# Kernel optimization log

Hardware: AMD Instinct MI355X
Metric: run time of the kernel (lower is better)

## Reference

```python
import jax, jax.numpy as jnp
import numpy as np

NHEAD = 8
TEMP = 1.0
LAMB = 1.0
G_MIN = 1e-3


def _linear(x, w, b):
    # torch nn.Linear convention: w is (out, in)
    return x @ w.T + b


def _ln(x, s, b):
    m = x.mean(-1, keepdims=True)
    v = ((x - m) ** 2).mean(-1, keepdims=True)
    return (x - m) / jnp.sqrt(v + 1e-5) * s + b


def _gate(x, w, b):
    # UncertaintyGate, gate_mode='mu_times_evi'
    nig = _linear(x, w, b)  # [B, L, 4]
    mu = nig[..., 0]
    v = jax.nn.softplus(nig[..., 1]) + 1e-6
    alpha = jax.nn.softplus(nig[..., 2]) + 1.0 + 1e-6
    beta = jax.nn.softplus(nig[..., 3]) + 1e-6
    sigma_e2 = beta / (v * (alpha - 1.0))
    g = jax.nn.sigmoid(mu) * jnp.exp(-LAMB * sigma_e2)
    return jnp.clip(g, G_MIN, 1.0)  # [B, L]


def _cross_attn(q, k, v, gate, mask):
    B, Lq, D = q.shape
    Lk = k.shape[1]
    hd = D // NHEAD
    q = q.reshape(B, Lq, NHEAD, hd).transpose(0, 2, 1, 3)
    k = k.reshape(B, Lk, NHEAD, hd).transpose(0, 2, 1, 3)
    v = v.reshape(B, Lk, NHEAD, hd).transpose(0, 2, 1, 3)
    scores = jnp.einsum('bhqd,bhkd->bhqk', q, k) / jnp.sqrt(jnp.float32(hd))
    scores = scores + jnp.log(gate + 1e-9)[:, None, None, :]  # per-key log-gate bias
    scores = jnp.where(mask[:, None, None, :] == 0, -1e9, scores)
    attn = jax.nn.softmax(scores / TEMP, axis=-1)
    out = jnp.einsum('bhqk,bhkd->bhqd', attn, v)
    return out.transpose(0, 2, 1, 3).reshape(B, Lq, D)


def _ffn(x, w1, b1, w2, b2):
    return _linear(jax.nn.gelu(_linear(x, w1, b1), approximate=False), w2, b2)


def setup_inputs() -> dict:
    key = jax.random.key(0)
    ks = iter(jax.random.split(key, 64))
    D, B, Ld, Lp = 512, 16, 256, 1024
    def w(shape, s=0.02):
        return jax.random.normal(next(ks), shape, jnp.float32) * s
    inp = {
        'h_d': jax.random.normal(next(ks), (B, Ld, D), jnp.float32),
        'h_p': jax.random.normal(next(ks), (B, Lp, D), jnp.float32),
        'gd_w': w((4, D)), 'gd_b': jnp.zeros((4,), jnp.float32),
        'gp_w': w((4, D)), 'gp_b': jnp.zeros((4,), jnp.float32),
        'wqd_w': w((D, D)), 'wqd_b': jnp.zeros((D,), jnp.float32),
        'wkp_w': w((D, D)), 'wkp_b': jnp.zeros((D,), jnp.float32),
        'wvp_w': w((D, D)), 'wvp_b': jnp.zeros((D,), jnp.float32),
        'wqp_w': w((D, D)), 'wqp_b': jnp.zeros((D,), jnp.float32),
        'wkd_w': w((D, D)), 'wkd_b': jnp.zeros((D,), jnp.float32),
        'wvd_w': w((D, D)), 'wvd_b': jnp.zeros((D,), jnp.float32),
        'od_w': w((D, D)), 'od_b': jnp.zeros((D,), jnp.float32),
        'op_w': w((D, D)), 'op_b': jnp.zeros((D,), jnp.float32),
        'fd1_w': w((4 * D, D)), 'fd1_b': jnp.zeros((4 * D,), jnp.float32),
        'fd2_w': w((D, 4 * D)), 'fd2_b': jnp.zeros((D,), jnp.float32),
        'fp1_w': w((4 * D, D)), 'fp1_b': jnp.zeros((4 * D,), jnp.float32),
        'fp2_w': w((D, 4 * D)), 'fp2_b': jnp.zeros((D,), jnp.float32),
        'nd1_s': jnp.ones((D,), jnp.float32), 'nd1_b': jnp.zeros((D,), jnp.float32),
        'nd2_s': jnp.ones((D,), jnp.float32), 'nd2_b': jnp.zeros((D,), jnp.float32),
        'np1_s': jnp.ones((D,), jnp.float32), 'np1_b': jnp.zeros((D,), jnp.float32),
        'np2_s': jnp.ones((D,), jnp.float32), 'np2_b': jnp.zeros((D,), jnp.float32),
        'mask_d': jnp.ones((B, Ld), jnp.int32),
        'mask_p': jnp.ones((B, Lp), jnp.int32),
    }
    return inp


def reference(h_d, h_p, gd_w, gd_b, gp_w, gp_b, wqd_w, wqd_b, wkp_w, wkp_b,
              wvp_w, wvp_b, wqp_w, wqp_b, wkd_w, wkd_b, wvd_w, wvd_b,
              od_w, od_b, op_w, op_b, fd1_w, fd1_b, fd2_w, fd2_b,
              fp1_w, fp1_b, fp2_w, fp2_b, nd1_s, nd1_b, nd2_s, nd2_b,
              np1_s, np1_b, np2_s, np2_b, mask_d, mask_p):
    # gates are computed from the ORIGINAL inputs
    g_d = _gate(h_d, gd_w, gd_b)
    g_p = _gate(h_p, gp_w, gp_b)
    # drug attends to protein
    attn_d = _cross_attn(_linear(h_d, wqd_w, wqd_b),
                         _linear(h_p, wkp_w, wkp_b),
                         _linear(h_p, wvp_w, wvp_b), g_p, mask_p)
    h_d = _ln(h_d + _linear(attn_d, od_w, od_b), nd1_s, nd1_b)
    # protein attends to UPDATED drug (matches original control flow)
    attn_p = _cross_attn(_linear(h_p, wqp_w, wqp_b),
                         _linear(h_d, wkd_w, wkd_b),
                         _linear(h_d, wvd_w, wvd_b), g_d, mask_d)
    h_p = _ln(h_p + _linear(attn_p, op_w, op_b), np1_s, np1_b)
    h_d = _ln(h_d + _ffn(h_d, fd1_w, fd1_b, fd2_w, fd2_b), nd2_s, nd2_b)
    h_p = _ln(h_p + _ffn(h_p, fp1_w, fp1_b, fp2_w, fp2_b), np2_s, np2_b)
    return (h_d, h_p)
```

## Files before the change

kernel.cpp:

```cpp
#include <hip/hip_runtime.h>

typedef float f32x4 __attribute__((ext_vector_type(4)));
typedef short bfrag __attribute__((ext_vector_type(8)));
typedef short s16x8 __attribute__((ext_vector_type(8)));
typedef unsigned short u16;

__device__ __forceinline__ u16 f2bf(float f) {
  union { float f; unsigned u; } x; x.f = f;
  unsigned r = x.u + 0x7fffu + ((x.u >> 16) & 1u);
  return (u16)(r >> 16);
}
__device__ __forceinline__ float bf2f(u16 v) {
  union { unsigned u; float f; } x; x.u = ((unsigned)v) << 16;
  return x.f;
}

__device__ __forceinline__ void g2l16(const void* g, void* l) {
  void* gnc = const_cast<void*>(g);
  __builtin_amdgcn_global_load_lds((__attribute__((address_space(1))) void*)gnc,
                                   (__attribute__((address_space(3))) void*)l, 16, 0, 0);
}

__device__ __forceinline__ f32x4 mfma16(bfrag a, bfrag b, f32x4 c) {
  asm volatile("v_mfma_f32_16x16x32_bf16 %0, %1, %2, %0" : "+v"(c) : "v"(a), "v"(b));
  return c;
}

__device__ __forceinline__ float wred_sum(float s) {
  #pragma unroll
  for (int o = 32; o; o >>= 1) s += __shfl_xor(s, o);
  return s;
}

__device__ __forceinline__ float gelu_f(float v) {
  return 0.5f * v * (1.f + erff(v * 0.70710678118f));
}

struct CvtArgs {
  const float* s[14];
  u16* d[14];
  int eb[14];
};

__global__ __launch_bounds__(256) void cvt_all(CvtArgs a) {
  const int blk = blockIdx.x;
  int base = 0;
  const float* sp = a.s[0];
  u16* dp = a.d[0];
  #pragma unroll
  for (int i = 0; i < 13; ++i) {
    if (blk >= a.eb[i]) { base = a.eb[i]; sp = a.s[i + 1]; dp = a.d[i + 1]; }
  }
  const size_t gi = ((size_t)(blk - base) * 256 + threadIdx.x) * 4;
  float4 f = *(const float4*)(sp + gi);
  ushort4 o;
  o.x = f2bf(f.x); o.y = f2bf(f.y); o.z = f2bf(f.z); o.w = f2bf(f.w);
  *(ushort4*)(dp + gi) = o;
}

__global__ __launch_bounds__(512) void biascat_k(
    const float* __restrict__ bkp, const float* __restrict__ bvp,
    const float* __restrict__ bqp, const float* __restrict__ bkd,
    const float* __restrict__ bvd, float* __restrict__ bp3,
    float* __restrict__ bd2) {
  int t = threadIdx.x;
  bp3[t] = bkp[t];
  bp3[512 + t] = bvp[t];
  bp3[1024 + t] = bqp[t];
  bd2[t] = bkd[t];
  bd2[512 + t] = bvd[t];
}

__device__ __forceinline__ float softplus_s(float x) {
  return fmaxf(x, 0.f) + log1pf(expf(-fabsf(x)));
}

__global__ __launch_bounds__(256) void gate_k(
    const float* __restrict__ hd, const float* __restrict__ hp,
    const float* __restrict__ wd, const float* __restrict__ bd,
    const float* __restrict__ wp, const float* __restrict__ bp,
    float* __restrict__ lgd, float* __restrict__ lgp, int mdTok) {
  const int lane = threadIdx.x & 63, wv = threadIdx.x >> 6;
  size_t tok = (size_t)blockIdx.x * 4 + wv;
  const float* h; const float* w4; const float* b4; float* lg;
  if (tok < (size_t)mdTok) { h = hd; w4 = wd; b4 = bd; lg = lgd; }
  else { h = hp; w4 = wp; b4 = bp; lg = lgp; tok -= mdTok; }
  const float* x = h + tok * 512;
  float s0 = 0.f, s1 = 0.f, s2 = 0.f, s3 = 0.f;
  #pragma unroll
  for (int i = 0; i < 8; ++i) {
    int c = (i << 6) + lane;
    float xv = x[c];
    s0 += xv * w4[c];
    s1 += xv * w4[512 + c];
    s2 += xv * w4[1024 + c];
    s3 += xv * w4[1536 + c];
  }
  s0 = wred_sum(s0); s1 = wred_sum(s1); s2 = wred_sum(s2); s3 = wred_sum(s3);
  if (lane == 0) {
    float mu = s0 + b4[0];
    float va = softplus_s(s1 + b4[1]) + 1e-6f;
    float al = softplus_s(s2 + b4[2]) + 1.f + 1e-6f;
    float be = softplus_s(s3 + b4[3]) + 1e-6f;
    float se2 = be / (va * (al - 1.f));
    float g = (1.f / (1.f + expf(-mu))) * expf(-se2);
    g = fminf(fmaxf(g, 1e-3f), 1.f);
    lg[tok] = logf(g + 1e-9f);
  }
}

template <int OUT>
__global__ __launch_bounds__(256) void ln_k(const u16* __restrict__ res,
                                            const u16* __restrict__ y,
                                            const float* __restrict__ sc,
                                            const float* __restrict__ bi,
                                            void* __restrict__ outv) {
  const int lane = threadIdx.x & 63, w = threadIdx.x >> 6;
  const size_t row = (size_t)blockIdx.x * 4 + w;
  const int c0 = lane * 8;
  float v[8];
  s16x8 yv = *(const s16x8*)(y + row * 512 + c0);
  s16x8 rv = *(const s16x8*)(res + row * 512 + c0);
  float s = 0.f;
  #pragma unroll
  for (int i = 0; i < 8; ++i) {
    v[i] = bf2f((u16)rv[i]) + bf2f((u16)yv[i]);
    s += v[i];
  }
  s = wred_sum(s);
  float m = s * (1.f / 512.f);
  float s2 = 0.f;
  #pragma unroll
  for (int i = 0; i < 8; ++i) { float d = v[i] - m; s2 += d * d; }
  s2 = wred_sum(s2);
  float inv = rsqrtf(s2 * (1.f / 512.f) + 1e-5f);
  float4 sc0 = *(const float4*)(sc + c0), sc1 = *(const float4*)(sc + c0 + 4);
  float4 bi0 = *(const float4*)(bi + c0), bi1 = *(const float4*)(bi + c0 + 4);
  float scv[8] = {sc0.x, sc0.y, sc0.z, sc0.w, sc1.x, sc1.y, sc1.z, sc1.w};
  float biv[8] = {bi0.x, bi0.y, bi0.z, bi0.w, bi1.x, bi1.y, bi1.z, bi1.w};
  float o[8];
  #pragma unroll
  for (int i = 0; i < 8; ++i) o[i] = (v[i] - m) * inv * scv[i] + biv[i];
  if constexpr (OUT == 0) {
    float* of = (float*)outv + row * 512 + c0;
    *(float4*)of = float4{o[0], o[1], o[2], o[3]};
    *(float4*)(of + 4) = float4{o[4], o[5], o[6], o[7]};
  } else {
    s16x8 ov;
    #pragma unroll
    for (int i = 0; i < 8; ++i) ov[i] = (short)f2bf(o[i]);
    *(s16x8*)((u16*)outv + row * 512 + c0) = ov;
  }
}

template <int KT>
__global__ __launch_bounds__(256) void flash_k(
    const u16* __restrict__ Q, const u16* __restrict__ Kv,
    const u16* __restrict__ Vt, const float* __restrict__ logg,
    const int* __restrict__ mask, u16* __restrict__ Out,
    int Lq, int Lk, float scale) {
  __shared__ __align__(16) u16 Kl[KT * 64];
  __shared__ __align__(16) u16 Vl[64 * KT];
  __shared__ __align__(16) u16 Pl[64 * (KT + 8)];
  const int tid = threadIdx.x;
  const int lane = tid & 63, wv = tid >> 6;
  const int lr = lane & 15, lg4 = lane >> 4;
  const int bh = blockIdx.z;
  const int b = bh >> 3, h = bh & 7;
  const int q0 = blockIdx.x * 64;

  bfrag af[2];
  {
    const u16* qrow = Q + (size_t)(b * Lq + q0 + wv * 16 + lr) * 512 + h * 64;
    af[0] = *(const bfrag*)(qrow + lg4 * 8);
    af[1] = *(const bfrag*)(qrow + 32 + lg4 * 8);
  }
  float mreg[4] = {-3e38f, -3e38f, -3e38f, -3e38f};
  float lreg[4] = {0.f, 0.f, 0.f, 0.f};
  f32x4 Oa[4] = {};
  const float* lgb = logg + (size_t)b * Lk;
  const int* mkb = mask + (size_t)b * Lk;

  const int NKT = Lk / KT;
  for (int t = 0; t < NKT; ++t) {
    const int k0 = t * KT;
    __syncthreads();
    {
      const char* kb = (const char*)(Kv + (size_t)(b * Lk + k0) * 512 + h * 64);
      #pragma unroll
      for (int r = 0; r < KT / 32; ++r) {
        int o = r * 4096 + tid * 16;
        int rr = o >> 7, cd = (o >> 4) & 7;
        int cs = cd ^ (rr & 7);
        g2l16(kb + (size_t)rr * 1024 + cs * 16, (char*)Kl + o);
      }
      const char* vb = (const char*)(Vt + (size_t)bh * 64 * Lk + k0);
      #pragma unroll
      for (int r = 0; r < KT / 32; ++r) {
        int o = r * 4096 + tid * 16;
        int rr = o >> 8, cd = (o >> 4) & 15;
        int cs = (cd & 8) | ((cd & 7) ^ (rr & 7));
        g2l16(vb + (size_t)rr * (Lk * 2) + cs * 16, (char*)Vl + o);
      }
    }
    __syncthreads();

    f32x4 sa[KT / 16];
    #pragma unroll
    for (int n = 0; n < KT / 16; ++n) {
      sa[n] = f32x4{0.f, 0.f, 0.f, 0.f};
      int row = n * 16 + lr;
      #pragma unroll
      for (int ks = 0; ks < 2; ++ks) {
        bfrag kf = *(const bfrag*)(Kl + row * 64 + (((ks * 4 + lg4) ^ (row & 7)) * 8));
        sa[n] = mfma16(af[ks], kf, sa[n]);
      }
    }
    asm volatile("s_nop 7\n\ts_nop 7");

    float pv[KT / 16][4];
    float nm[4] = {-3e38f, -3e38f, -3e38f, -3e38f};
    #pragma unroll
    for (int n = 0; n < KT / 16; ++n) {
      int kk = k0 + n * 16 + lr;
      float lgv = lgb[kk];
      int mkv = mkb[kk];
      #pragma unroll
      for (int e = 0; e < 4; ++e) {
        float tv = mkv ? fmaf(sa[n][e], scale, lgv) : -1e9f;
        pv[n][e] = tv;
        nm[e] = fmaxf(nm[e], tv);
      }
    }
    float fac[4], rs[4];
    #pragma unroll
    for (int e = 0; e < 4; ++e) {
      nm[e] = fmaxf(nm[e], __shfl_xor(nm[e], 1));
      nm[e] = fmaxf(nm[e], __shfl_xor(nm[e], 2));
      nm[e] = fmaxf(nm[e], __shfl_xor(nm[e], 4));
      nm[e] = fmaxf(nm[e], __shfl_xor(nm[e], 8));
      nm[e] = fmaxf(nm[e], mreg[e]);
      fac[e] = __expf(mreg[e] - nm[e]);
      mreg[e] = nm[e];
      rs[e] = 0.f;
    }
    #pragma unroll
    for (int n = 0; n < KT / 16; ++n)
      #pragma unroll
      for (int e = 0; e < 4; ++e) {
        float p = __expf(pv[n][e] - nm[e]);
        pv[n][e] = p;
        rs[e] += p;
      }
    #pragma unroll
    for (int e = 0; e < 4; ++e) {
      rs[e] += __shfl_xor(rs[e], 1);
      rs[e] += __shfl_xor(rs[e], 2);
      rs[e] += __shfl_xor(rs[e], 4);
      rs[e] += __shfl_xor(rs[e], 8);
      lreg[e] = lreg[e] * fac[e] + rs[e];
    }
    #pragma unroll
    for (int n2 = 0; n2 < 4; ++n2)
      #pragma unroll
      for (int e = 0; e < 4; ++e) Oa[n2][e] *= fac[e];

    {
      int prow = wv * 16 + lg4 * 4;
      #pragma unroll
      for (int n = 0; n < KT / 16; ++n)
        #pragma unroll
        for (int e = 0; e < 4; ++e)
          Pl[(prow + e) * (KT + 8) + n * 16 + lr] = f2bf(pv[n][e]);
    }
    #pragma unroll
    for (int ks = 0; ks < KT / 32; ++ks) {
      bfrag pf = *(const bfrag*)(Pl + (wv * 16 + lr) * (KT + 8) + (ks * 4 + lg4) * 8);
      #pragma unroll
      for (int n2 = 0; n2 < 4; ++n2) {
        int vrow = n2 * 16 + lr;
        int ch = ks * 4 + lg4;
        int chs = (ch & 8) | ((ch & 7) ^ (vrow & 7));
        bfrag vf = *(const bfrag*)(Vl + vrow * KT + chs * 8);
        Oa[n2] = mfma16(pf, vf, Oa[n2]);
      }
    }
  }
  asm volatile("s_nop 7\n\ts_nop 7");

  float inv[4];
  #pragma unroll
  for (int e = 0; e < 4; ++e) inv[e] = 1.f / lreg[e];
  u16* ob = Out + (size_t)(b * Lq + q0 + wv * 16 + lg4 * 4) * 512 + h * 64;
  #pragma unroll
  for (int n2 = 0; n2 < 4; ++n2)
    #pragma unroll
    for (int e = 0; e < 4; ++e)
      ob[(size_t)e * 512 + n2 * 16 + lr] = f2bf(Oa[n2][e] * inv[e]);
}

template <int FM, int FN, int EPI>
__global__ __launch_bounds__(256) void gemm_k(
    const u16* __restrict__ A, const u16* __restrict__ W,
    const float* __restrict__ bias, void* __restrict__ C, void* __restrict__ C2,
    void* __restrict__ C3, int K, int lda, int ldw, int ldc, int NB, int TR) {
  constexpr int BM = 2 * FM * 16;
  constexpr int BN = 2 * FN * 16;
  __shared__ __align__(16) u16 Al[BM * 64];
  __shared__ __align__(16) u16 Wl[BN * 64];
  const int tid = threadIdx.x;
  const int qq = gridDim.x >> 3;
  const int wg = (blockIdx.x & 7) * qq + (blockIdx.x >> 3);
  const int bx = wg % NB, by = wg / NB;
  const int row0 = by * BM, col0 = bx * BN;
  const int lane = tid & 63, wv = tid >> 6;
  const int wr = wv >> 1, wc = wv & 1;
  const int rowW = wr * FM * 16, colW = wc * FN * 16;
  const int lr = lane & 15, lg4 = lane >> 4;

  const u16* aSrc[BM / 32];
  const u16* wSrc[BN / 32];
  int aDst[BM / 32], wDst[BN / 32];
  #pragma unroll
  for (int r = 0; r < BM / 32; ++r) {
    int o = r * 4096 + tid * 16;
    int arow = o >> 7, cd = (o >> 4) & 7, cs = cd ^ (arow & 7);
    aSrc[r] = A + (size_t)(row0 + arow) * lda + cs * 8;
    aDst[r] = o;
  }
  #pragma unroll
  for (int r = 0; r < BN / 32; ++r) {
    int o = r * 4096 + tid * 16;
    int wrow = o >> 7, cd = (o >> 4) & 7, cs = cd ^ (wrow & 7);
    wSrc[r] = W + (size_t)(col0 + wrow) * ldw + cs * 8;
    wDst[r] = o;
  }
  int aOff[FM][2], wOff[FN][2];
  #pragma unroll
  for (int m = 0; m < FM; ++m) {
    int rowi = rowW + m * 16 + lr;
    #pragma unroll
    for (int ks = 0; ks < 2; ++ks)
      aOff[m][ks] = rowi * 64 + (((ks * 4 + lg4) ^ (rowi & 7)) * 8);
  }
  #pragma unroll
  for (int n = 0; n < FN; ++n) {
    int rowi = colW + n * 16 + lr;
    #pragma unroll
    for (int ks = 0; ks < 2; ++ks)
      wOff[n][ks] = rowi * 64 + (((ks * 4 + lg4) ^ (rowi & 7)) * 8);
  }

  f32x4 acc[FM][FN] = {};

  for (int k0 = 0; k0 < K; k0 += 64) {
    #pragma unroll
    for (int r = 0; r < BM / 32; ++r) g2l16(aSrc[r] + k0, (char*)Al + aDst[r]);
    #pragma unroll
    for (int r = 0; r < BN / 32; ++r) g2l16(wSrc[r] + k0, (char*)Wl + wDst[r]);
    __syncthreads();
    #pragma unroll
    for (int ks = 0; ks < 2; ++ks) {
      bfrag af[FM], wf[FN];
      #pragma unroll
      for (int m = 0; m < FM; ++m) af[m] = *(const bfrag*)(Al + aOff[m][ks]);
      #pragma unroll
      for (int n = 0; n < FN; ++n) wf[n] = *(const bfrag*)(Wl + wOff[n][ks]);
      #pragma unroll
      for (int m = 0; m < FM; ++m)
        #pragma unroll
        for (int n = 0; n < FN; ++n) acc[m][n] = mfma16(af[m], wf[n], acc[m][n]);
    }
    if (k0 + 64 < K) __syncthreads();
  }
  asm volatile("s_nop 7\n\ts_nop 7\n\ts_nop 7");

  #pragma unroll
  for (int m = 0; m < FM; ++m) {
    #pragma unroll
    for (int n = 0; n < FN; ++n) {
      int rb = row0 + rowW + m * 16 + lg4 * 4;
      int c = col0 + colW + n * 16 + lr;
      float bv = bias[c];
      if constexpr (EPI == 1) {
        u16* Cu = (u16*)C;
        #pragma unroll
        for (int e = 0; e < 4; ++e)
          Cu[(size_t)(rb + e) * ldc + c] = f2bf(acc[m][n][e] + bv);
      } else if constexpr (EPI == 2) {
        u16* Cu = (u16*)C;
        #pragma unroll
        for (int e = 0; e < 4; ++e)
          Cu[(size_t)(rb + e) * ldc + c] = f2bf(gelu_f(acc[m][n][e] + bv));
      } else if constexpr (EPI == 4) {
        if (c < 512) {
          u16* Cu = (u16*)C;
          #pragma unroll
          for (int e = 0; e < 4; ++e)
            Cu[(size_t)(rb + e) * 512 + c] = f2bf(acc[m][n][e] + bv);
        } else if (c < 1024) {
          u16* Cu = (u16*)C2;
          int cl = c - 512;
          int b2 = rb / TR, j0 = rb - b2 * TR;
          int h2 = cl >> 6, dd = cl & 63;
          ushort4 pk;
          pk.x = f2bf(acc[m][n][0] + bv);
          pk.y = f2bf(acc[m][n][1] + bv);
          pk.z = f2bf(acc[m][n][2] + bv);
          pk.w = f2bf(acc[m][n][3] + bv);
          *(ushort4*)&Cu[(((size_t)b2 * 8 + h2) * 64 + dd) * TR + j0] = pk;
        } else {
          u16* Cu = (u16*)C3;
          int cl = c - 1024;
          #pragma unroll
          for (int e = 0; e < 4; ++e)
            Cu[(size_t)(rb + e) * 512 + cl] = f2bf(acc[m][n][e] + bv);
        }
      } else {
        if (c < 512) {
          u16* Cu = (u16*)C;
          #pragma unroll
          for (int e = 0; e < 4; ++e)
            Cu[(size_t)(rb + e) * ldc + c] = f2bf(acc[m][n][e] + bv);
        } else {
          u16* Cu = (u16*)C2;
          int cl = c - 512;
          int b2 = rb / TR, j0 = rb - b2 * TR;
          int h2 = cl >> 6, dd = cl & 63;
          ushort4 pk;
          pk.x = f2bf(acc[m][n][0] + bv);
          pk.y = f2bf(acc[m][n][1] + bv);
          pk.z = f2bf(acc[m][n][2] + bv);
          pk.w = f2bf(acc[m][n][3] + bv);
          *(ushort4*)&Cu[(((size_t)b2 * 8 + h2) * 64 + dd) * TR + j0] = pk;
        }
      }
    }
  }
}

extern "C" void kernel_launch(void* const* d_in, const int* in_sizes, int n_in,
                              void* d_out, int out_size, void* d_ws, size_t ws_size,
                              hipStream_t stream) {
  const float* h_d = (const float*)d_in[0];
  const float* h_p = (const float*)d_in[1];
  const float* gd_w = (const float*)d_in[2];
  const float* gd_b = (const float*)d_in[3];
  const float* gp_w = (const float*)d_in[4];
  const float* gp_b = (const float*)d_in[5];
  const float* wqd_w = (const float*)d_in[6];  const float* wqd_b = (const float*)d_in[7];
  const float* wkp_w = (const float*)d_in[8];  const float* wkp_b = (const float*)d_in[9];
  const float* wvp_w = (const float*)d_in[10]; const float* wvp_b = (const float*)d_in[11];
  const float* wqp_w = (const float*)d_in[12]; const float* wqp_b = (const float*)d_in[13];
  const float* wkd_w = (const float*)d_in[14]; const float* wkd_b = (const float*)d_in[15];
  const float* wvd_w = (const float*)d_in[16]; const float* wvd_b = (const float*)d_in[17];
  const float* od_w = (const float*)d_in[18];  const float* od_b = (const float*)d_in[19];
  const float* op_w = (const float*)d_in[20];  const float* op_b = (const float*)d_in[21];
  const float* fd1_w = (const float*)d_in[22]; const float* fd1_b = (const float*)d_in[23];
  const float* fd2_w = (const float*)d_in[24]; const float* fd2_b = (const float*)d_in[25];
  const float* fp1_w = (const float*)d_in[26]; const float* fp1_b = (const float*)d_in[27];
  const float* fp2_w = (const float*)d_in[28]; const float* fp2_b = (const float*)d_in[29];
  const float* nd1_s = (const float*)d_in[30]; const float* nd1_b = (const float*)d_in[31];
  const float* nd2_s = (const float*)d_in[32]; const float* nd2_b = (const float*)d_in[33];
  const float* np1_s = (const float*)d_in[34]; const float* np1_b = (const float*)d_in[35];
  const float* np2_s = (const float*)d_in[36]; const float* np2_b = (const float*)d_in[37];
  const int* mask_d = (const int*)d_in[38];
  const int* mask_p = (const int*)d_in[39];

  constexpr int B = 16, Ld = 256, Lp = 1024, D = 512, H = 8, F = 2048;
  constexpr int Md = B * Ld;
  constexpr int Mp = B * Lp;
  constexpr int BH = B * H;

  char* ws = (char*)d_ws;
  size_t off = 0;
  auto alloc = [&](size_t bytes) {
    size_t o = off;
    off += (bytes + 255) & ~(size_t)255;
    return o;
  };
  auto a16 = [&](size_t els) { return (u16*)(ws + alloc(els * 2)); };
  auto a32 = [&](size_t els) { return (float*)(ws + alloc(els * 4)); };

  u16* w_qd = a16((size_t)D * D);
  u16* w_kp = a16((size_t)D * D);
  u16* w_vp = a16((size_t)D * D);
  u16* w_qp = a16((size_t)D * D);
  u16* w_kd = a16((size_t)D * D);
  u16* w_vd = a16((size_t)D * D);
  u16* w_od = a16((size_t)D * D);
  u16* w_op = a16((size_t)D * D);
  u16* w_fd1 = a16((size_t)F * D);
  u16* w_fd2 = a16((size_t)F * D);
  u16* w_fp1 = a16((size_t)F * D);
  u16* w_fp2 = a16((size_t)F * D);

  u16* hd16 = a16((size_t)Md * D);
  u16* hd2_16 = a16((size_t)Md * D);
  u16* hp16 = a16((size_t)Mp * D);
  u16* qd16 = a16((size_t)Md * D);
  u16* kp16 = a16((size_t)Mp * D);
  u16* qp16 = a16((size_t)Mp * D);
  u16* vt16 = a16((size_t)Mp * D);
  u16* obuf16 = a16((size_t)Mp * D);
  u16* t16 = a16((size_t)Mp * F);
  float* logg_d = a32(Md);
  float* logg_p = a32(Mp);
  float* bp3 = a32(1536);
  float* bd2 = a32(1024);

  {
    CvtArgs a;
    const float* src[14] = {h_d, h_p, wqd_w, wkp_w, wvp_w, wqp_w, wkd_w,
                            wvd_w, od_w, op_w, fd1_w, fd2_w, fp1_w, fp2_w};
    u16* dst[14] = {hd16, hp16, w_qd, w_kp, w_vp, w_qp, w_kd,
                    w_vd, w_od, w_op, w_fd1, w_fd2, w_fp1, w_fp2};
    const int nelem[14] = {Md * D, Mp * D, D * D, D * D, D * D, D * D, D * D,
                           D * D, D * D, D * D, F * D, F * D, F * D, F * D};
    int pfx = 0;
    for (int i = 0; i < 14; ++i) {
      a.s[i] = src[i];
      a.d[i] = dst[i];
      pfx += nelem[i] / 1024;
      a.eb[i] = pfx;
    }
    cvt_all<<<pfx, 256, 0, stream>>>(a);
  }
  biascat_k<<<1, 512, 0, stream>>>(wkp_b, wvp_b, wqp_b, wkd_b, wvd_b, bp3, bd2);

  gate_k<<<(Md + Mp) / 4, 256, 0, stream>>>(h_d, h_p, gd_w, gd_b, gp_w, gp_b,
                                            logg_d, logg_p, Md);

  gemm_k<4, 4, 4><<<(Mp / 128) * (1536 / 128), 256, 0, stream>>>(
      hp16, w_kp, bp3, kp16, vt16, qp16, D, D, D, D, 1536 / 128, Lp);

  gemm_k<4, 4, 1><<<(Md / 128) * (D / 128), 256, 0, stream>>>(
      hd16, w_qd, wqd_b, qd16, nullptr, nullptr, D, D, D, D, D / 128, 0);

  flash_k<128><<<dim3(Ld / 64, 1, BH), 256, 0, stream>>>(
      qd16, kp16, vt16, logg_p, mask_p, qd16, Ld, Lp, 0.125f);

  gemm_k<4, 4, 1><<<(Md / 128) * (D / 128), 256, 0, stream>>>(
      qd16, w_od, od_b, obuf16, nullptr, nullptr, D, D, D, D, D / 128, 0);
  ln_k<1><<<Md / 4, 256, 0, stream>>>(hd16, obuf16, nd1_s, nd1_b, hd2_16);

  gemm_k<4, 4, 5><<<(Md / 128) * (1024 / 128), 256, 0, stream>>>(
      hd2_16, w_kd, bd2, qd16, vt16, nullptr, D, D, D, D, 1024 / 128, Ld);

  flash_k<128><<<dim3(Lp / 64, 1, BH), 256, 0, stream>>>(
      qp16, qd16, vt16, logg_d, mask_d, qp16, Lp, Ld, 0.125f);

  gemm_k<4, 4, 1><<<(Mp / 128) * (D / 128), 256, 0, stream>>>(
      qp16, w_op, op_b, obuf16, nullptr, nullptr, D, D, D, D, D / 128, 0);
  ln_k<1><<<Mp / 4, 256, 0, stream>>>(hp16, obuf16, np1_s, np1_b, hp16);

  gemm_k<4, 4, 2><<<(Md / 128) * (F / 128), 256, 0, stream>>>(
      hd2_16, w_fd1, fd1_b, t16, nullptr, nullptr, D, D, D, F, F / 128, 0);
  gemm_k<4, 4, 1><<<(Md / 128) * (D / 128), 256, 0, stream>>>(
      t16, w_fd2, fd2_b, obuf16, nullptr, nullptr, F, F, F, D, D / 128, 0);
  ln_k<0><<<Md / 4, 256, 0, stream>>>(hd2_16, obuf16, nd2_s, nd2_b, (float*)d_out);

  gemm_k<4, 4, 2><<<(Mp / 128) * (F / 128), 256, 0, stream>>>(
      hp16, w_fp1, fp1_b, t16, nullptr, nullptr, D, D, D, F, F / 128, 0);
  gemm_k<4, 4, 1><<<(Mp / 128) * (D / 128), 256, 0, stream>>>(
      t16, w_fp2, fp2_b, obuf16, nullptr, nullptr, F, F, F, D, D / 128, 0);
  ln_k<0><<<Mp / 4, 256, 0, stream>>>(hp16, obuf16, np2_s, np2_b,
                                      (float*)d_out + (size_t)Md * D);
}
```

Before: 396.5 us.

## Batch independent GEMMs into grouped launches and fuse final LayerNorms

Replaces the templated GEMM with a runtime descriptor-driven kernel that can run two independent GEMMs in one grid. Groups KVQ with Qd, Kd/Vd with the drug FFN1, and protein FFN1 with drug FFN2, and merges the two final LayerNorms into one launch. The aim is fewer launches and better CU fill on small GEMMs. It also shrinks the K-tile from 64 to 32 with a new swizzle, which means more barriers per K step, and moves the epilogue choice to runtime branches.

New measurement: 422.1 us. +6.5%, slower.

```diff
diff --git a/kernel.cpp b/kernel.cpp
--- a/kernel.cpp
+++ b/kernel.cpp
@@ -109,14 +109,10 @@
   }
 }
 
-template <int OUT>
-__global__ __launch_bounds__(256) void ln_k(const u16* __restrict__ res,
-                                            const u16* __restrict__ y,
-                                            const float* __restrict__ sc,
-                                            const float* __restrict__ bi,
-                                            void* __restrict__ outv) {
-  const int lane = threadIdx.x & 63, w = threadIdx.x >> 6;
-  const size_t row = (size_t)blockIdx.x * 4 + w;
+__device__ __forceinline__ void ln_body(const u16* res, const u16* y,
+                                        const float* sc, const float* bi,
+                                        void* outv, int fp32out, size_t row,
+                                        int lane) {
   const int c0 = lane * 8;
   float v[8];
   s16x8 yv = *(const s16x8*)(y + row * 512 + c0);
@@ -141,7 +137,7 @@
   float o[8];
   #pragma unroll
   for (int i = 0; i < 8; ++i) o[i] = (v[i] - m) * inv * scv[i] + biv[i];
-  if constexpr (OUT == 0) {
+  if (fp32out) {
     float* of = (float*)outv + row * 512 + c0;
     *(float4*)of = float4{o[0], o[1], o[2], o[3]};
     *(float4*)(of + 4) = float4{o[4], o[5], o[6], o[7]};
@@ -151,6 +147,31 @@
     for (int i = 0; i < 8; ++i) ov[i] = (short)f2bf(o[i]);
     *(s16x8*)((u16*)outv + row * 512 + c0) = ov;
   }
+}
+
+__global__ __launch_bounds__(256) void ln_k(const u16* __restrict__ res,
+                                            const u16* __restrict__ y,
+                                            const float* __restrict__ sc,
+                                            const float* __restrict__ bi,
+                                            u16* __restrict__ out) {
+  const int lane = threadIdx.x & 63, w = threadIdx.x >> 6;
+  const size_t row = (size_t)blockIdx.x * 4 + w;
+  ln_body(res, y, sc, bi, out, 0, row, lane);
+}
+
+__global__ __launch_bounds__(256) void lnf_k(
+    const u16* __restrict__ rd, const u16* __restrict__ yd,
+    const float* __restrict__ scd, const float* __restrict__ bid,
+    float* __restrict__ od,
+    const u16* __restrict__ rp, const u16* __restrict__ yp,
+    const float* __restrict__ scp, const float* __restrict__ bip,
+    float* __restrict__ op, int mdRows) {
+  const int lane = threadIdx.x & 63, w = threadIdx.x >> 6;
+  size_t row = (size_t)blockIdx.x * 4 + w;
+  if (row < (size_t)mdRows)
+    ln_body(rd, yd, scd, bid, od, 1, row, lane);
+  else
+    ln_body(rp, yp, scp, bip, op, 1, row - mdRows, lane);
 }
 
 template <int KT>
@@ -299,140 +320,123 @@
       ob[(size_t)e * 512 + n2 * 16 + lr] = f2bf(Oa[n2][e] * inv[e]);
 }
 
-template <int FM, int FN, int EPI>
-__global__ __launch_bounds__(256) void gemm_k(
-    const u16* __restrict__ A, const u16* __restrict__ W,
-    const float* __restrict__ bias, void* __restrict__ C, void* __restrict__ C2,
-    void* __restrict__ C3, int K, int lda, int ldw, int ldc, int NB, int TR) {
-  constexpr int BM = 2 * FM * 16;
-  constexpr int BN = 2 * FN * 16;
-  __shared__ __align__(16) u16 Al[BM * 64];
-  __shared__ __align__(16) u16 Wl[BN * 64];
+struct GemmDesc {
+  const u16* A;
+  const u16* W;
+  const float* bias;
+  u16 *C, *C2, *C3;
+  int K, lda, ldw, ldc, NB, TR, epi, nblocks;
+};
+
+__global__ __launch_bounds__(256) void gemm_k(GemmDesc d0, GemmDesc d1) {
+  __shared__ __align__(16) u16 Al[128 * 32];
+  __shared__ __align__(16) u16 Wl[128 * 32];
   const int tid = threadIdx.x;
   const int qq = gridDim.x >> 3;
-  const int wg = (blockIdx.x & 7) * qq + (blockIdx.x >> 3);
-  const int bx = wg % NB, by = wg / NB;
-  const int row0 = by * BM, col0 = bx * BN;
+  int wg = (blockIdx.x & 7) * qq + (blockIdx.x >> 3);
+  const GemmDesc& d = (wg < d0.nblocks) ? d0 : d1;
+  if (wg >= d0.nblocks) wg -= d0.nblocks;
+  const int bx = wg % d.NB, by = wg / d.NB;
+  const int row0 = by * 128, col0 = bx * 128;
   const int lane = tid & 63, wv = tid >> 6;
   const int wr = wv >> 1, wc = wv & 1;
-  const int rowW = wr * FM * 16, colW = wc * FN * 16;
+  const int rowW = wr * 64, colW = wc * 64;
   const int lr = lane & 15, lg4 = lane >> 4;
-
-  const u16* aSrc[BM / 32];
-  const u16* wSrc[BN / 32];
-  int aDst[BM / 32], wDst[BN / 32];
-  #pragma unroll
-  for (int r = 0; r < BM / 32; ++r) {
+  const int K = d.K;
+
+  const u16* aSrc[2];
+  const u16* wSrc[2];
+  int aDst[2], wDst[2];
+  #pragma unroll
+  for (int r = 0; r < 2; ++r) {
     int o = r * 4096 + tid * 16;
-    int arow = o >> 7, cd = (o >> 4) & 7, cs = cd ^ (arow & 7);
-    aSrc[r] = A + (size_t)(row0 + arow) * lda + cs * 8;
+    int row = o >> 6, cd = (o >> 4) & 3, cs = cd ^ ((row >> 1) & 3);
+    aSrc[r] = d.A + (size_t)(row0 + row) * d.lda + cs * 8;
+    wSrc[r] = d.W + (size_t)(col0 + row) * d.ldw + cs * 8;
     aDst[r] = o;
-  }
-  #pragma unroll
-  for (int r = 0; r < BN / 32; ++r) {
-    int o = r * 4096 + tid * 16;
-    int wrow = o >> 7, cd = (o >> 4) & 7, cs = cd ^ (wrow & 7);
-    wSrc[r] = W + (size_t)(col0 + wrow) * ldw + cs * 8;
     wDst[r] = o;
   }
-  int aOff[FM][2], wOff[FN][2];
-  #pragma unroll
-  for (int m = 0; m < FM; ++m) {
+  int aOff[4], wOff[4];
+  #pragma unroll
+  for (int m = 0; m < 4; ++m) {
     int rowi = rowW + m * 16 + lr;
-    #pragma unroll
-    for (int ks = 0; ks < 2; ++ks)
-      aOff[m][ks] = rowi * 64 + (((ks * 4 + lg4) ^ (rowi & 7)) * 8);
-  }
-  #pragma unroll
-  for (int n = 0; n < FN; ++n) {
-    int rowi = colW + n * 16 + lr;
-    #pragma unroll
-    for (int ks = 0; ks < 2; ++ks)
-      wOff[n][ks] = rowi * 64 + (((ks * 4 + lg4) ^ (rowi & 7)) * 8);
-  }
-
-  f32x4 acc[FM][FN] = {};
-
-  for (int k0 = 0; k0 < K; k0 += 64) {
-    #pragma unroll
-    for (int r = 0; r < BM / 32; ++r) g2l16(aSrc[r] + k0, (char*)Al + aDst[r]);
-    #pragma unroll
-    for (int r = 0; r < BN / 32; ++r) g2l16(wSrc[r] + k0, (char*)Wl + wDst[r]);
+    aOff[m] = rowi * 32 + ((lg4 ^ ((rowi >> 1) & 3)) * 8);
+    int rowj = colW + m * 16 + lr;
+    wOff[m] = rowj * 32 + ((lg4 ^ ((rowj >> 1) & 3)) * 8);
+  }
+
+  f32x4 acc[4][4] = {};
+
+  for (int k0 = 0; k0 < K; k0 += 32) {
+    #pragma unroll
+    for (int r = 0; r < 2; ++r) g2l16(aSrc[r] + k0, (char*)Al + aDst[r]);
+    #pragma unroll
+    for (int r = 0; r < 2; ++r) g2l16(wSrc[r] + k0, (char*)Wl + wDst[r]);
     __syncthreads();
-    #pragma unroll
-    for (int ks = 0; ks < 2; ++ks) {
-      bfrag af[FM], wf[FN];
-      #pragma unroll
-      for (int m = 0; m < FM; ++m) af[m] = *(const bfrag*)(Al + aOff[m][ks]);
-      #pragma unroll
-      for (int n = 0; n < FN; ++n) wf[n] = *(const bfrag*)(Wl + wOff[n][ks]);
-      #pragma unroll
-      for (int m = 0; m < FM; ++m)
-        #pragma unroll
-        for (int n = 0; n < FN; ++n) acc[m][n] = mfma16(af[m], wf[n], acc[m][n]);
-    }
-    if (k0 + 64 < K) __syncthreads();
+    bfrag af[4], wf[4];
+    #pragma unroll
+    for (int m = 0; m < 4; ++m) af[m] = *(const bfrag*)(Al + aOff[m]);
+    #pragma unroll
+    for (int n = 0; n < 4; ++n) wf[n] = *(const bfrag*)(Wl + wOff[n]);
+    #pragma unroll
+    for (int m = 0; m < 4; ++m)
+      #pragma unroll
+      for (int n = 0; n < 4; ++n) acc[m][n] = mfma16(af[m], wf[n], acc[m][n]);
+    if (k0 + 32 < K) __syncthreads();
   }
   asm volatile("s_nop 7\n\ts_nop 7\n\ts_nop 7");
 
   #pragma unroll
-  for (int m = 0; m < FM; ++m) {
-    #pragma unroll
-    for (int n = 0; n < FN; ++n) {
+  for (int m = 0; m < 4; ++m) {
+    #pragma unroll
+    for (int n = 0; n < 4; ++n) {
       int rb = row0 + rowW + m * 16 + lg4 * 4;
       int c = col0 + colW + n * 16 + lr;
-      float bv = bias[c];
-      if constexpr (EPI == 1) {
-        u16* Cu = (u16*)C;
+      float bv = d.bias[c];
+      if (d.epi == 1) {
         #pragma unroll
         for (int e = 0; e < 4; ++e)
-          Cu[(size_t)(rb + e) * ldc + c] = f2bf(acc[m][n][e] + bv);
-      } else if constexpr (EPI == 2) {
-        u16* Cu = (u16*)C;
+          d.C[(size_t)(rb + e) * d.ldc + c] = f2bf(acc[m][n][e] + bv);
+      } else if (d.epi == 2) {
         #pragma unroll
         for (int e = 0; e < 4; ++e)
-          Cu[(size_t)(rb + e) * ldc + c] = f2bf(gelu_f(acc[m][n][e] + bv));
-      } else if constexpr (EPI == 4) {
+          d.C[(size_t)(rb + e) * d.ldc + c] = f2bf(gelu_f(acc[m][n][e] + bv));
+      } else if (d.epi == 4) {
         if (c < 512) {
-          u16* Cu = (u16*)C;
           #pragma unroll
           for (int e = 0; e < 4; ++e)
-            Cu[(size_t)(rb + e) * 512 + c] = f2bf(acc[m][n][e] + bv);
+            d.C[(size_t)(rb + e) * 512 + c] = f2bf(acc[m][n][e] + bv);
         } else if (c < 1024) {
-          u16* Cu = (u16*)C2;
           int cl = c - 512;
-          int b2 = rb / TR, j0 = rb - b2 * TR;
+          int b2 = rb / d.TR, j0 = rb - b2 * d.TR;
           int h2 = cl >> 6, dd = cl & 63;
           ushort4 pk;
           pk.x = f2bf(acc[m][n][0] + bv);
           pk.y = f2bf(acc[m][n][1] + bv);
           pk.z = f2bf(acc[m][n][2] + bv);
           pk.w = f2bf(acc[m][n][3] + bv);
-          *(ushort4*)&Cu[(((size_t)b2 * 8 + h2) * 64 + dd) * TR + j0] = pk;
+          *(ushort4*)&d.C2[(((size_t)b2 * 8 + h2) * 64 + dd) * d.TR + j0] = pk;
         } else {
-          u16* Cu = (u16*)C3;
           int cl = c - 1024;
           #pragma unroll
           for (int e = 0; e < 4; ++e)
-            Cu[(size_t)(rb + e) * 512 + cl] = f2bf(acc[m][n][e] + bv);
+            d.C3[(size_t)(rb + e) * 512 + cl] = f2bf(acc[m][n][e] + bv);
         }
       } else {
         if (c < 512) {
-          u16* Cu = (u16*)C;
           #pragma unroll
           for (int e = 0; e < 4; ++e)
-            Cu[(size_t)(rb + e) * ldc + c] = f2bf(acc[m][n][e] + bv);
+            d.C[(size_t)(rb + e) * d.ldc + c] = f2bf(acc[m][n][e] + bv);
         } else {
-          u16* Cu = (u16*)C2;
           int cl = c - 512;
-          int b2 = rb / TR, j0 = rb - b2 * TR;
+          int b2 = rb / d.TR, j0 = rb - b2 * d.TR;
           int h2 = cl >> 6, dd = cl & 63;
           ushort4 pk;
           pk.x = f2bf(acc[m][n][0] + bv);
           pk.y = f2bf(acc[m][n][1] + bv);
           pk.z = f2bf(acc[m][n][2] + bv);
           pk.w = f2bf(acc[m][n][3] + bv);
-          *(ushort4*)&Cu[(((size_t)b2 * 8 + h2) * 64 + dd) * TR + j0] = pk;
+          *(ushort4*)&d.C2[(((size_t)b2 * 8 + h2) * 64 + dd) * d.TR + j0] = pk;
         }
       }
     }
@@ -503,7 +507,9 @@
   u16* qp16 = a16((size_t)Mp * D);
   u16* vt16 = a16((size_t)Mp * D);
   u16* obuf16 = a16((size_t)Mp * D);
+  u16* obuf_d = a16((size_t)Md * D);
   u16* t16 = a16((size_t)Mp * F);
+  u16* t16d = a16((size_t)Md * F);
   float* logg_d = a32(Md);
   float* logg_p = a32(Mp);
   float* bp3 = a32(1536);
@@ -531,39 +537,59 @@
   gate_k<<<(Md + Mp) / 4, 256, 0, stream>>>(h_d, h_p, gd_w, gd_b, gp_w, gp_b,
                                             logg_d, logg_p, Md);
 
-  gemm_k<4, 4, 4><<<(Mp / 128) * (1536 / 128), 256, 0, stream>>>(
-      hp16, w_kp, bp3, kp16, vt16, qp16, D, D, D, D, 1536 / 128, Lp);
-
-  gemm_k<4, 4, 1><<<(Md / 128) * (D / 128), 256, 0, stream>>>(
-      hd16, w_qd, wqd_b, qd16, nullptr, nullptr, D, D, D, D, D / 128, 0);
+  GemmDesc none = {};
+
+  {
+    GemmDesc kvq = {hp16, w_kp, bp3, kp16, vt16, qp16,
+                    D, D, D, D, 1536 / 128, Lp, 4, (Mp / 128) * (1536 / 128)};
+    GemmDesc qd = {hd16, w_qd, wqd_b, qd16, nullptr, nullptr,
+                   D, D, D, D, D / 128, 0, 1, (Md / 128) * (D / 128)};
+    gemm_k<<<kvq.nblocks + qd.nblocks, 256, 0, stream>>>(kvq, qd);
+  }
 
   flash_k<128><<<dim3(Ld / 64, 1, BH), 256, 0, stream>>>(
       qd16, kp16, vt16, logg_p, mask_p, qd16, Ld, Lp, 0.125f);
 
-  gemm_k<4, 4, 1><<<(Md / 128) * (D / 128), 256, 0, stream>>>(
-      qd16, w_od, od_b, obuf16, nullptr, nullptr, D, D, D, D, D / 128, 0);
-  ln_k<1><<<Md / 4, 256, 0, stream>>>(hd16, obuf16, nd1_s, nd1_b, hd2_16);
-
-  gemm_k<4, 4, 5><<<(Md / 128) * (1024 / 128), 256, 0, stream>>>(
-      hd2_16, w_kd, bd2, qd16, vt16, nullptr, D, D, D, D, 1024 / 128, Ld);
+  {
+    GemmDesc od = {qd16, w_od, od_b, obuf_d, nullptr, nullptr,
+                   D, D, D, D, D / 128, 0, 1, (Md / 128) * (D / 128)};
+    gemm_k<<<od.nblocks, 256, 0, stream>>>(od, none);
+  }
+  ln_k<<<Md / 4, 256, 0, stream>>>(hd16, obuf_d, nd1_s, nd1_b, hd2_16);
+
+  {
+    GemmDesc kdvd = {hd2_16, w_kd, bd2, qd16, vt16, nullptr,
+                     D, D, D, D, 1024 / 128, Ld, 5, (Md / 128) * (1024 / 128)};
+    GemmDesc fd1 = {hd2_16, w_fd1, fd1_b, t16d, nullptr, nullptr,
+                    D, D, D, F, F / 128, 0, 2, (Md / 128) * (F / 128)};
+    gemm_k<<<kdvd.nblocks + fd1.nblocks, 256, 0, stream>>>(kdvd, fd1);
+  }
 
   flash_k<128><<<dim3(Lp / 64, 1, BH), 256, 0, stream>>>(
       qp16, qd16, vt16, logg_d, mask_d, qp16, Lp, Ld, 0.125f);
 
-  gemm_k<4, 4, 1><<<(Mp / 128) * (D / 128), 256, 0, stream>>>(
-      qp16, w_op, op_b, obuf16, nullptr, nullptr, D, D, D, D, D / 128, 0);
-  ln_k<1><<<Mp / 4, 256, 0, stream>>>(hp16, obuf16, np1_s, np1_b, hp16);
-
-  gemm_k<4, 4, 2><<<(Md / 128) * (F / 128), 256, 0, stream>>>(
-      hd2_16, w_fd1, fd1_b, t16, nullptr, nullptr, D, D, D, F, F / 128, 0);
-  gemm_k<4, 4, 1><<<(Md / 128) * (D / 128), 256, 0, stream>>>(
-      t16, w_fd2, fd2_b, obuf16, nullptr, nullptr, F, F, F, D, D / 128, 0);
-  ln_k<0><<<Md / 4, 256, 0, stream>>>(hd2_16, obuf16, nd2_s, nd2_b, (float*)d_out);
-
-  gemm_k<4, 4, 2><<<(Mp / 128) * (F / 128), 256, 0, stream>>>(
-      hp16, w_fp1, fp1_b, t16, nullptr, nullptr, D, D, D, F, F / 128, 0);
-  gemm_k<4, 4, 1><<<(Mp / 128) * (D / 128), 256, 0, stream>>>(
-      t16, w_fp2, fp2_b, obuf16, nullptr, nullptr, F, F, F, D, D / 128, 0);
-  ln_k<0><<<Mp / 4, 256, 0, stream>>>(hp16, obuf16, np2_s, np2_b,
-                                      (float*)d_out + (size_t)Md * D);
-}
+  {
+    GemmDesc op = {qp16, w_op, op_b, obuf16, nullptr, nullptr,
+                   D, D, D, D, D / 128, 0, 1, (Mp / 128) * (D / 128)};
+    gemm_k<<<op.nblocks, 256, 0, stream>>>(op, none);
+  }
+  ln_k<<<Mp / 4, 256, 0, stream>>>(hp16, obuf16, np1_s, np1_b, hp16);
+
+  {
+    GemmDesc fp1 = {hp16, w_fp1, fp1_b, t16, nullptr, nullptr,
+                    D, D, D, F, F / 128, 0, 2, (Mp / 128) * (F / 128)};
+    GemmDesc fd2 = {t16d, w_fd2, fd2_b, obuf_d, nullptr, nullptr,
+                    F, F, F, D, D / 128, 0, 1, (Md / 128) * (D / 128)};
+    gemm_k<<<fp1.nblocks + fd2.nblocks, 256, 0, stream>>>(fp1, fd2);
+  }
+
+  {
+    GemmDesc fp2 = {t16, w_fp2, fp2_b, obuf16, nullptr, nullptr,
+                    F, F, F, D, D / 128, 0, 1, (Mp / 128) * (D / 128)};
+    gemm_k<<<fp2.nblocks, 256, 0, stream>>>(fp2, none);
+  }
+
+  lnf_k<<<(Md + Mp) / 4, 256, 0, stream>>>(
+      hd2_16, obuf_d, nd2_s, nd2_b, (float*)d_out,
+      hp16, obuf16, np2_s, np2_b, (float*)d_out + (size_t)Md * D, Md);
+}
```
